# Kernel optimization log

Hardware: AMD Instinct MI355X
Metric: run time of the kernel (lower is better)

## Reference

```python
import jax, jax.numpy as jnp
import numpy as np

B, T, S_ENC, D = 2, 1024, 1024, 2048
NQ, NKV, H = 16, 8, 256
EPS = 1e-6
CAP = 50.0
SCALE = 0.0625  # query_pre_attn_scalar = head_dim**-0.5
BASE = 10000
K_MASK = -2.3819763e+38


def rms_norm(x, scale, eps=EPS):
    var = jnp.mean(jnp.square(x), axis=-1, keepdims=True)
    return x * jax.lax.rsqrt(var + eps) * (1.0 + scale)


def apply_rope(x, positions, base=BASE):
    # x: [B, L, N, H], positions: [B, L] float. rope_proportion=1.0 -> full head.
    head_dim = x.shape[-1]
    timescale = base ** (2.0 / head_dim * jnp.arange(head_dim // 2, dtype=jnp.float32))
    sinusoid = positions[..., None] / timescale  # [B, L, H/2]
    sinusoid = sinusoid[..., None, :]            # [B, L, 1, H/2]
    sin, cos = jnp.sin(sinusoid), jnp.cos(sinusoid)
    x1, x2 = jnp.split(x, 2, axis=-1)
    return jnp.concatenate([x1 * cos - x2 * sin, x2 * cos + x1 * sin], axis=-1).astype(x.dtype)


def setup_inputs() -> dict:
    key = jax.random.key(0)
    ks = jax.random.split(key, 6)
    hidden_states = jax.random.normal(ks[0], (B, T, D), jnp.float32)
    encoder_hidden_states = jax.random.normal(ks[1], (B, S_ENC, D), jnp.float32)
    position_ids = jnp.broadcast_to(jnp.arange(T, dtype=jnp.int32), (B, T))
    causal = jnp.tril(jnp.ones((T, T), bool))
    merged = jnp.concatenate([causal, jnp.ones((T, S_ENC), bool)], axis=-1)
    merged_attention_mask = jnp.broadcast_to(merged[None, None], (B, 1, T, T + S_ENC))
    q_w = jax.random.normal(ks[2], (NQ, D, H), jnp.float32) * 0.02
    k_w = jax.random.normal(ks[3], (NKV, D, H), jnp.float32) * 0.02
    v_w = jax.random.normal(ks[4], (NKV, D, H), jnp.float32) * 0.02
    o_w = jax.random.normal(ks[5], (NQ, H, D), jnp.float32) * 0.02
    q_scale = jnp.zeros((H,), jnp.float32)
    k_scale = jnp.zeros((H,), jnp.float32)
    return {
        'hidden_states': hidden_states,
        'encoder_hidden_states': encoder_hidden_states,
        'position_ids': position_ids,
        'merged_attention_mask': merged_attention_mask,
        'q_w': q_w, 'k_w': k_w, 'v_w': v_w, 'o_w': o_w,
        'q_scale': q_scale, 'k_scale': k_scale,
    }


def reference(hidden_states, encoder_hidden_states, position_ids, merged_attention_mask,
              q_w, k_w, v_w, o_w, q_scale, k_scale):
    # Fused QKV projections
    q = jnp.einsum('BTD,NDH->BTNH', hidden_states, q_w)
    self_k = jnp.einsum('BTD,NDH->BTNH', hidden_states, k_w)
    self_v = jnp.einsum('BTD,NDH->BTNH', hidden_states, v_w)
    # QK RMSNorm
    q = rms_norm(q, q_scale)
    self_k = rms_norm(self_k, k_scale)
    # RoPE on decoder-side q/k only
    pos = position_ids.astype(jnp.float32)
    q = apply_rope(q, pos)
    self_k = apply_rope(self_k, pos)
    # Cross KV (no RoPE, k-norm applied)
    cross_k = rms_norm(jnp.einsum('BTD,NDH->BTNH', encoder_hidden_states, k_w), k_scale)
    cross_v = jnp.einsum('BTD,NDH->BTNH', encoder_hidden_states, v_w)
    # Merge KV: [B, T+S_enc, NKV, H]
    k = jnp.concatenate([self_k, cross_k], axis=1)
    v = jnp.concatenate([self_v, cross_v], axis=1)
    q = q * SCALE
    # GQA: group query heads over kv heads
    G = NQ // NKV
    qg = q.reshape(B, T, NKV, G, H)
    logits = jnp.einsum('BTKGH,BSKH->BKGTS', qg, k)
    # Logit soft-cap
    logits = CAP * jnp.tanh(logits / CAP)
    mask = merged_attention_mask[:, 0][:, None, None]  # [B,1,1,T,S_comb]
    logits = jnp.where(mask, logits, K_MASK)
    probs = jax.nn.softmax(logits, axis=-1)
    out = jnp.einsum('BKGTS,BSKH->BTKGH', probs, v).reshape(B, T, NQ, H)
    return jnp.einsum('BTNH,NHD->BTD', out, o_w)
```

## Files before the change

### kernel.cpp

```cpp
#include <hip/hip_runtime.h>
#include <hip/hip_bf16.h>
#include <stdint.h>

typedef __hip_bfloat16 bf16;
typedef __attribute__((ext_vector_type(8))) short bv8;
typedef __attribute__((ext_vector_type(4))) float f32x4;


__device__ __forceinline__ f32x4 mfma16(bv8 a, bv8 b, f32x4 c) {
  return __builtin_amdgcn_mfma_f32_16x16x32_bf16(a, b, c, 0, 0, 0);
}

__device__ __forceinline__ void gload16(const void* g, void* lds) {
  __builtin_amdgcn_global_load_lds((const __attribute__((address_space(1))) void*)g,
                                   (__attribute__((address_space(3))) void*)lds, 16, 0, 0);
}

__device__ __forceinline__ void storeC(float* p, float v) { *p = v; }
__device__ __forceinline__ void storeC(bf16* p, float v) { *p = __float2bfloat16(v); }

__global__ void cast2_f32_bf16(const float* __restrict__ a, const float* __restrict__ b,
                               bf16* __restrict__ da, bf16* __restrict__ db, int n4each) {
  int i = blockIdx.x * blockDim.x + threadIdx.x;
  const float* s;
  bf16* d;
  if (i < n4each) { s = a; d = da; }
  else            { s = b; d = db; i -= n4each; }
  float4 v = reinterpret_cast<const float4*>(s)[i];
  bf16 t[4] = {__float2bfloat16(v.x), __float2bfloat16(v.y),
               __float2bfloat16(v.z), __float2bfloat16(v.w)};
  reinterpret_cast<uint64_t*>(d)[i] = *reinterpret_cast<uint64_t*>(t);
}

__global__ void transpose_all(const float* __restrict__ q_w, const float* __restrict__ k_w,
                              const float* __restrict__ v_w, const float* __restrict__ o_w,
                              bf16* __restrict__ wqkvt, bf16* __restrict__ owt) {
  __shared__ float tile[32][33];
  const int bid = blockIdx.x;
  const float* s;
  bf16* d;
  int R, C, c0, r0;
  if (bid < 16384) {
    const int z = bid >> 9;
    const int rem = bid & 511;
    s = (z < 16) ? q_w + (size_t)z * 524288
      : (z < 24) ? k_w + (size_t)(z - 16) * 524288
                 : v_w + (size_t)(z - 24) * 524288;
    d = wqkvt + (size_t)z * 524288;
    R = 2048; C = 256;
    c0 = (rem & 7) * 32; r0 = (rem >> 3) * 32;
  } else {
    const int rem = bid - 16384;
    s = o_w; d = owt;
    R = 4096; C = 2048;
    c0 = (rem & 63) * 32; r0 = (rem >> 6) * 32;
  }
  const int x = threadIdx.x, y = threadIdx.y;
#pragma unroll
  for (int i = 0; i < 32; i += 8)
    tile[y + i][x] = s[(size_t)(r0 + y + i) * C + c0 + x];
  __syncthreads();
#pragma unroll
  for (int i = 0; i < 32; i += 8)
    d[(size_t)(c0 + y + i) * R + r0 + x] = __float2bfloat16(tile[x][y + i]);
}

__global__ void transpose_v2(const bf16* __restrict__ vself, const bf16* __restrict__ vcross,
                             bf16* __restrict__ dst) {
  __shared__ bf16 tile[32][33];
  const int z = blockIdx.z;
  const int zz = z & 15, b = zz >> 3, kvh = zz & 7;
  const bool cross = z >= 16;
  const bf16* srcb = cross ? vcross : vself;
  const int src_ld = cross ? 4096 : 8192;
  const int t0 = cross ? 1024 : 0;
  const bf16* s = srcb + (size_t)(b * 1024) * src_ld + kvh * 256;
  bf16* d = dst + (size_t)(zz * 256) * 2048 + t0;
  const int h0 = blockIdx.x * 32, tt0 = blockIdx.y * 32;
  const int x = threadIdx.x, y = threadIdx.y;
#pragma unroll
  for (int i = 0; i < 32; i += 8)
    tile[y + i][x] = s[(size_t)(tt0 + y + i) * src_ld + h0 + x];
  __syncthreads();
#pragma unroll
  for (int i = 0; i < 32; i += 8)
    d[(size_t)(h0 + y + i) * 2048 + tt0 + x] = tile[x][y + i];
}

template <typename CT>
__device__ __forceinline__ void gemm_body(const bf16* __restrict__ A, const bf16* __restrict__ Bt,
                                          CT* __restrict__ C, int N, int K,
                                          int m0, int n0, int kbase, int ksteps) {
  __shared__ __align__(16) bf16 As[128 * 32];
  __shared__ __align__(16) bf16 Bs[128 * 32];
  const int tid = threadIdx.x;
  const int w = tid >> 6, l = tid & 63;
  const int wr = w >> 1, wc = w & 1;
  const int l15 = l & 15, lhi = l >> 4;
  const bf16* ag = A + (size_t)(m0 + (tid >> 2)) * K + kbase + (tid & 3) * 8;
  const bf16* bg = Bt + (size_t)(n0 + (tid >> 2)) * K + kbase + (tid & 3) * 8;
  bf16* asw = As + w * 512;
  bf16* bsw = Bs + w * 512;
  f32x4 acc[4][4] = {};
  for (int k0 = 0; k0 < ksteps; k0 += 32) {
    gload16(ag + k0, asw);
    gload16(ag + (size_t)64 * K + k0, asw + 2048);
    gload16(bg + k0, bsw);
    gload16(bg + (size_t)64 * K + k0, bsw + 2048);
    asm volatile("s_waitcnt vmcnt(0)" ::: "memory");
    __syncthreads();
    bv8 af[4], bfv[4];
#pragma unroll
    for (int m = 0; m < 4; ++m)
      af[m] = *reinterpret_cast<const bv8*>(As + (wr * 64 + m * 16 + l15) * 32 + lhi * 8);
#pragma unroll
    for (int n = 0; n < 4; ++n)
      bfv[n] = *reinterpret_cast<const bv8*>(Bs + (wc * 64 + n * 16 + l15) * 32 + lhi * 8);
#pragma unroll
    for (int m = 0; m < 4; ++m)
#pragma unroll
      for (int n = 0; n < 4; ++n)
        acc[m][n] = mfma16(af[m], bfv[n], acc[m][n]);
    __syncthreads();
  }
  const int r0 = m0 + wr * 64 + lhi * 4;
  const int c0 = n0 + wc * 64 + l15;
#pragma unroll
  for (int m = 0; m < 4; ++m)
#pragma unroll
    for (int n = 0; n < 4; ++n) {
      f32x4 v = acc[m][n];
#pragma unroll
      for (int j = 0; j < 4; ++j)
        storeC(&C[(size_t)(r0 + m * 16 + j) * N + c0 + n * 16], v[j]);
    }
}

__launch_bounds__(256)
__global__ void gemm_proj(const bf16* __restrict__ hid, const bf16* __restrict__ enc,
                          const bf16* __restrict__ wqkvt, bf16* __restrict__ cself,
                          bf16* __restrict__ ccross) {
  const int bx = blockIdx.x;
  const bool cross = bx >= 64;
  const bf16* A = cross ? enc : hid;
  const bf16* Bt = cross ? wqkvt + 8388608 : wqkvt;
  bf16* C = cross ? ccross : cself;
  const int N = cross ? 4096 : 8192;
  const int n0 = (cross ? bx - 64 : bx) * 128;
  gemm_body<bf16>(A, Bt, C, N, 2048, blockIdx.y * 128, n0, 0, 2048);
}

__launch_bounds__(256)
__global__ void gemm_osplit(const bf16* __restrict__ A, const bf16* __restrict__ Bt,
                            float* __restrict__ out, float* __restrict__ p1,
                            float* __restrict__ p2, float* __restrict__ p3) {
  const int z = blockIdx.z;
  float* C = (z == 0) ? out : (z == 1) ? p1 : (z == 2) ? p2 : p3;
  gemm_body<float>(A, Bt, C, 2048, 4096, blockIdx.y * 128, blockIdx.x * 128,
                   z * 1024, 1024);
}

__global__ void add_inplace4(float* __restrict__ out, const float* __restrict__ p1,
                             const float* __restrict__ p2, const float* __restrict__ p3,
                             int n4) {
  int i = blockIdx.x * blockDim.x + threadIdx.x;
  if (i >= n4) return;
  float4 a = reinterpret_cast<float4*>(out)[i];
  float4 b = reinterpret_cast<const float4*>(p1)[i];
  float4 c = reinterpret_cast<const float4*>(p2)[i];
  float4 d = reinterpret_cast<const float4*>(p3)[i];
  a.x += b.x + c.x + d.x;
  a.y += b.y + c.y + d.y;
  a.z += b.z + c.z + d.z;
  a.w += b.w + c.w + d.w;
  reinterpret_cast<float4*>(out)[i] = a;
}

__launch_bounds__(256)
__global__ void norm_all(const bf16* __restrict__ cself, const bf16* __restrict__ ccross,
                         const float* __restrict__ q_s, const float* __restrict__ k_s,
                         const int* __restrict__ pos_ids,
                         bf16* __restrict__ qb, bf16* __restrict__ kbuf) {
  const int rid = blockIdx.x * 4 + (threadIdx.x >> 6);
  const int l = threadIdx.x & 63;
  const bf16* src;
  const float* scale;
  bf16* dst;
  int r, src_ld, src_col0, nheads, dst_S, dst_t0;
  float mul;
  bool rope;
  if (rid < 32768) {
    r = rid; src = cself; src_ld = 8192; src_col0 = 0; scale = q_s;
    dst = qb; nheads = 16; dst_S = 1024; dst_t0 = 0; mul = 0.0625f; rope = true;
  } else if (rid < 49152) {
    r = rid - 32768; src = cself; src_ld = 8192; src_col0 = 4096; scale = k_s;
    dst = kbuf; nheads = 8; dst_S = 2048; dst_t0 = 0; mul = 1.0f; rope = true;
  } else {
    r = rid - 49152; src = ccross; src_ld = 4096; src_col0 = 0; scale = k_s;
    dst = kbuf; nheads = 8; dst_S = 2048; dst_t0 = 1024; mul = 1.0f; rope = false;
  }
  const int token = r / nheads;
  const int n = r - token * nheads;
  const int b = token >> 10;
  const int t = token & 1023;
  const size_t soff = (size_t)token * src_ld + src_col0 + n * 256 + l * 4;
  bf16 xb[4];
  *reinterpret_cast<uint64_t*>(xb) = *reinterpret_cast<const uint64_t*>(src + soff);
  float x[4];
#pragma unroll
  for (int c = 0; c < 4; ++c) x[c] = __bfloat162float(xb[c]);
  float ss = x[0] * x[0] + x[1] * x[1] + x[2] * x[2] + x[3] * x[3];
#pragma unroll
  for (int d = 1; d < 64; d <<= 1) ss += __shfl_xor(ss, d);
  const float rr = rsqrtf(ss * (1.0f / 256.0f) + 1e-6f);
  float v[4];
#pragma unroll
  for (int c = 0; c < 4; ++c) v[c] = x[c] * rr * (1.0f + scale[l * 4 + c]);
  if (rope) {
    const float pos = (float)pos_ids[token];
    float o[4];
#pragma unroll
    for (int c = 0; c < 4; ++c) {
      const int j = (l & 31) * 4 + c;
      const float inv_ts = exp2f(-(float)j * 0.10381025296523007f);
      const float arg = pos * inv_ts;
      const float sj = sinf(arg), cj = cosf(arg);
      const float partner = __shfl_xor(v[c], 32);
      o[c] = (l < 32) ? (v[c] * cj - partner * sj) : (v[c] * cj + partner * sj);
    }
#pragma unroll
    for (int c = 0; c < 4; ++c) v[c] = o[c];
  }
  bf16 ob[4];
#pragma unroll
  for (int c = 0; c < 4; ++c) ob[c] = __float2bfloat16(v[c] * mul);
  const size_t doff = ((size_t)((b * nheads + n) * dst_S + dst_t0 + t)) * 256 + l * 4;
  *reinterpret_cast<uint64_t*>(dst + doff) = *reinterpret_cast<uint64_t*>(ob);
}

__launch_bounds__(512, 2)
__global__ void attn_kernel(const bf16* __restrict__ qb, const bf16* __restrict__ kb,
                            const bf16* __restrict__ vt, bf16* __restrict__ attn_out) {
  __shared__ __align__(16) bf16 Ks[2][64 * 256];
  __shared__ __align__(16) bf16 Vs[2][256 * 64];
  __shared__ __align__(16) bf16 pbuf[2][64 * 72];
  __shared__ float rsb[2][4][2][4][4];
  const int lin = blockIdx.x + 16 * blockIdx.y;
  const int kvc = (lin & 7) | (((lin >> 7) & 1) << 3);
  const int p   = (lin >> 3) & 15;
  const int b = kvc >> 3, kvh = kvc & 7;
  const int tid = threadIdx.x, w = tid >> 6, l = tid & 63;
  const int g = w >> 2, i2 = (w >> 1) & 1, sh = w & 1, hq = w & 3;
  const int n = kvh * 2 + g;
  const int l15 = l & 15, lhi = l >> 4;
  const int xr = (l15 & 7) << 4;

  const int rA = p * 32, rB = (31 - p) * 32;
  const int ntSelf = ((31 - p) >> 1) + 1;
  const int nASelf = (p >> 1) + 1;
  const int nt = ntSelf + 16;

  const bf16* kbase = kb + (size_t)(b * 8 + kvh) * 2048 * 256;
  const bf16* vbase = vt + (size_t)(b * 8 + kvh) * 256 * 2048;

  const bf16* ksrc[4];
  const bf16* vsrc[4];
#pragma unroll
  for (int i = 0; i < 4; ++i) {
    const int r0 = (w * 4 + i) * 2 + (l >> 5);
    const int cbs = ((l & 31) * 16) ^ ((r0 & 7) << 4);
    ksrc[i] = kbase + r0 * 256 + (cbs >> 1);
    const int h0 = (w * 4 + i) * 8 + (l >> 3);
    const int cbv = ((l & 7) * 16) ^ ((h0 & 7) << 4);
    vsrc[i] = vbase + (size_t)h0 * 2048 + (cbv >> 1);
  }

  bv8 qf[2][8];
#pragma unroll
  for (int h = 0; h < 2; ++h) {
    const int rbase = (h ? rB : rA) + i2 * 16;
    const bf16* qp = qb + ((size_t)(b * 16 + n) * 1024 + rbase + l15) * 256 + lhi * 8;
#pragma unroll
    for (int f = 0; f < 8; ++f) qf[h][f] = *reinterpret_cast<const bv8*>(qp + f * 32);
  }

  f32x4 oacc[4][4] = {};
  float rs[2][4] = {};

#pragma unroll
  for (int i = 0; i < 4; ++i) gload16(ksrc[i], &Ks[0][(w * 4 + i) * 512]);
#pragma unroll
  for (int i = 0; i < 4; ++i) gload16(vsrc[i], &Vs[0][(w * 4 + i) * 512]);
  asm volatile("s_waitcnt vmcnt(0)" ::: "memory");
  __syncthreads();

  for (int it = 0; it < nt; ++it) {
    const int cur = it & 1;
    const int s0 = (it < ntSelf) ? it * 64 : 1024 + (it - ntSelf) * 64;
    const bool selfpart = it < ntSelf;
    const bool aAct = (it < nASelf) || !selfpart;
    if (it + 1 < nt) {
      const int itn = it + 1;
      const int s1 = (itn < ntSelf) ? itn * 64 : 1024 + (itn - ntSelf) * 64;
#pragma unroll
      for (int i = 0; i < 4; ++i)
        gload16(ksrc[i] + (size_t)s1 * 256, &Ks[cur ^ 1][(w * 4 + i) * 512]);
#pragma unroll
      for (int i = 0; i < 4; ++i)
        gload16(vsrc[i] + s1, &Vs[cur ^ 1][(w * 4 + i) * 512]);
    }
    f32x4 lacc[2][2] = {};
    __builtin_amdgcn_s_setprio(1);
#pragma unroll
    for (int ss2 = 0; ss2 < 2; ++ss2) {
      const int rbase = ((sh * 2 + ss2) * 16 + l15) * 256;
#pragma unroll
      for (int f = 0; f < 8; ++f) {
        const int off = rbase + (((f * 64 + lhi * 16) ^ xr) >> 1);
        bv8 kf = *reinterpret_cast<const bv8*>(&Ks[cur][off]);
        lacc[1][ss2] = mfma16(qf[1][f], kf, lacc[1][ss2]);
        if (aAct) lacc[0][ss2] = mfma16(qf[0][f], kf, lacc[0][ss2]);
      }
    }
    __builtin_amdgcn_s_setprio(0);
#pragma unroll
    for (int h = 0; h < 2; ++h) {
      if (h == 0 && !aAct) continue;
      const int slot = h ? (i2 + 2) : i2;
      const int rbase = (h ? rB : rA) + i2 * 16;
#pragma unroll
      for (int ss2 = 0; ss2 < 2; ++ss2)
#pragma unroll
        for (int j = 0; j < 4; ++j) {
          const float raw = lacc[h][ss2][j];
          const float e2 = __expf(raw * 0.04f);
          const int s_idx = s0 + (sh * 2 + ss2) * 16 + l15;
          const int trow = rbase + lhi * 4 + j;
          const bool ok = !selfpart || (s_idx <= trow);
          const float pv = ok ? __expf(50.f - __fdividef(100.f, e2 + 1.f)) : 0.f;
          rs[h][j] += pv;
          pbuf[g][(slot * 16 + lhi * 4 + j) * 72 + (sh * 2 + ss2) * 16 + l15] =
              __float2bfloat16(pv);
        }
    }
    __syncthreads();
    __builtin_amdgcn_s_setprio(1);
#pragma unroll
    for (int ks = 0; ks < 2; ++ks) {
      bv8 paB[2], paA[2];
#pragma unroll
      for (int q = 0; q < 2; ++q)
        paB[q] = *reinterpret_cast<const bv8*>(
            &pbuf[g][((2 + q) * 16 + l15) * 72 + ks * 32 + lhi * 8]);
      if (aAct)
#pragma unroll
        for (int q = 0; q < 2; ++q)
          paA[q] = *reinterpret_cast<const bv8*>(
              &pbuf[g][(q * 16 + l15) * 72 + ks * 32 + lhi * 8]);
#pragma unroll
      for (int i = 0; i < 4; ++i) {
        const int off = ((hq * 4 + i) * 16 + l15) * 64 + (((ks * 64 + lhi * 16) ^ xr) >> 1);
        bv8 vf = *reinterpret_cast<const bv8*>(&Vs[cur][off]);
        oacc[2][i] = mfma16(paB[0], vf, oacc[2][i]);
        oacc[3][i] = mfma16(paB[1], vf, oacc[3][i]);
        if (aAct) {
          oacc[0][i] = mfma16(paA[0], vf, oacc[0][i]);
          oacc[1][i] = mfma16(paA[1], vf, oacc[1][i]);
        }
      }
    }
    __builtin_amdgcn_s_setprio(0);
    asm volatile("s_waitcnt vmcnt(0)" ::: "memory");
    __syncthreads();
  }
#pragma unroll
  for (int h = 0; h < 2; ++h) {
    const int slot = h ? (i2 + 2) : i2;
#pragma unroll
    for (int j = 0; j < 4; ++j) {
      float s = rs[h][j];
      s += __shfl_xor(s, 1);
      s += __shfl_xor(s, 2);
      s += __shfl_xor(s, 4);
      s += __shfl_xor(s, 8);
      if (l15 == 0) rsb[g][slot][sh][j][lhi] = s;
    }
  }
  __syncthreads();
  const int rowb[4] = {rA, rA + 16, rB, rB + 16};
  bf16* op = attn_out + (size_t)(b * 1024) * 4096 + n * 256 + l15;
#pragma unroll
  for (int slot = 0; slot < 4; ++slot) {
    float invr[4];
#pragma unroll
    for (int j = 0; j < 4; ++j)
      invr[j] = 1.0f / (rsb[g][slot][0][j][lhi] + rsb[g][slot][1][j][lhi]);
#pragma unroll
    for (int i = 0; i < 4; ++i)
#pragma unroll
      for (int j = 0; j < 4; ++j)
        op[(size_t)(rowb[slot] + lhi * 4 + j) * 4096 + (hq * 4 + i) * 16] =
            __float2bfloat16(oacc[slot][i][j] * invr[j]);
  }
}

extern "C" void kernel_launch(void* const* d_in, const int* in_sizes, int n_in,
                              void* d_out, int out_size, void* d_ws, size_t ws_size,
                              hipStream_t stream) {
  (void)in_sizes; (void)n_in; (void)out_size; (void)ws_size;
  const float* hidden = (const float*)d_in[0];
  const float* enc    = (const float*)d_in[1];
  const int*   pos    = (const int*)d_in[2];
  const float* q_w = (const float*)d_in[4];
  const float* k_w = (const float*)d_in[5];
  const float* v_w = (const float*)d_in[6];
  const float* o_w = (const float*)d_in[7];
  const float* q_s = (const float*)d_in[8];
  const float* k_s = (const float*)d_in[9];
  float* out = (float*)d_out;

  char* base = (char*)d_ws;
  bf16* hid_b  = (bf16*)(base + 0);
  bf16* enc_b  = (bf16*)(base + 8388608);
  bf16* qb     = (bf16*)(base + 0);
  float* p2    = (float*)(base + 0);
  bf16* wqkvt  = (bf16*)(base + 16777216);
  bf16* kbuf   = (bf16*)(base + 16777216);
  float* p3    = (float*)(base + 16777216);
  bf16* vtb    = (bf16*)(base + 33554432);
  bf16* owt    = (bf16*)(base + 50331648);
  bf16* cself  = (bf16*)(base + 67108864);
  bf16* attn_b = (bf16*)(base + 67108864);
  float* p1    = (float*)(base + 83886080);
  bf16* ccross = (bf16*)(base + 100663296);

  dim3 tb32(32, 8);
  cast2_f32_bf16<<<8192, 256, 0, stream>>>(hidden, enc, hid_b, enc_b, 1048576);
  transpose_all<<<24576, tb32, 0, stream>>>(q_w, k_w, v_w, o_w, wqkvt, owt);
  gemm_proj<<<dim3(96, 16), 256, 0, stream>>>(hid_b, enc_b, wqkvt, cself, ccross);
  norm_all<<<16384, 256, 0, stream>>>(cself, ccross, q_s, k_s, pos, qb, kbuf);
  transpose_v2<<<dim3(8, 32, 32), tb32, 0, stream>>>(cself + 6144, ccross + 2048, vtb);
  attn_kernel<<<dim3(16, 16), 512, 0, stream>>>(qb, kbuf, vtb, attn_b);
  gemm_osplit<<<dim3(16, 16, 4), 256, 0, stream>>>(attn_b, owt, out, p1, p2, p3);
  add_inplace4<<<4096, 256, 0, stream>>>(out, p1, p2, p3, 1048576);
}
```

Baseline: 367.5 us.

## Replace projection GEMM with 256x256-tile pipelined kernel and XCD-aware block mapping

Replaces the 128x128-tile QKV projection GEMM with a 256x256-tile, 512-thread kernel. It double-buffers A and B tiles in swizzled LDS using direct global-to-LDS loads, and interleaves the B prefetch with the MFMA sub-phases under manual waitcnt, barriers and s_setprio. Block indices are remapped so each XCD works on a contiguous group of N tiles. The goal is more reuse per loaded byte and better L2 locality across XCDs, at the cost of more registers and LDS per block and fragile hand-written synchronisation.

```diff
diff --git a/kernel.cpp b/kernel.cpp
--- a/kernel.cpp
+++ b/kernel.cpp
@@ -136,18 +136,121 @@
     }
 }
 
-__launch_bounds__(256)
-__global__ void gemm_proj(const bf16* __restrict__ hid, const bf16* __restrict__ enc,
-                          const bf16* __restrict__ wqkvt, bf16* __restrict__ cself,
-                          bf16* __restrict__ ccross) {
-  const int bx = blockIdx.x;
-  const bool cross = bx >= 64;
-  const bf16* A = cross ? enc : hid;
-  const bf16* Bt = cross ? wqkvt + 8388608 : wqkvt;
-  bf16* C = cross ? ccross : cself;
-  const int N = cross ? 4096 : 8192;
-  const int n0 = (cross ? bx - 64 : bx) * 128;
-  gemm_body<bf16>(A, Bt, C, N, 2048, blockIdx.y * 128, n0, 0, 2048);
+__device__ __forceinline__ void stage_half(const bf16* __restrict__ G, int ldg, int row0,
+                                           int kcol0, bf16* lds, int tid) {
+#pragma unroll
+  for (int j = 0; j < 2; ++j) {
+    const int idx = tid + j * 512;
+    const int r = idx >> 3;
+    const int cb = ((idx & 7) * 16) ^ ((r & 7) << 4);
+    gload16(G + (size_t)(row0 + r) * ldg + kcol0 + (cb >> 1), lds + idx * 8);
+  }
+}
+
+__device__ __forceinline__ bv8 frag(const bf16* p, int row, int ks, int lhi, int xw) {
+  return *reinterpret_cast<const bv8*>(p + row * 64 + (((ks * 64 + lhi * 16) ^ xw) >> 1));
+}
+
+__launch_bounds__(512, 2)
+__global__ void gemm_proj256(const bf16* __restrict__ hid, const bf16* __restrict__ enc,
+                             const bf16* __restrict__ wqkvt, bf16* __restrict__ cself,
+                             bf16* __restrict__ ccross) {
+  __shared__ __align__(16) bf16 Al[2][2][128 * 64];
+  __shared__ __align__(16) bf16 Bl[2][2][128 * 64];
+  const int lin = blockIdx.x;
+  const int xcd = lin & 7, idx = lin >> 3;
+  const bf16* A;
+  const bf16* Bt;
+  bf16* C;
+  int N, M0, N0;
+  if (idx < 32) {
+    A = hid; Bt = wqkvt; C = cself; N = 8192;
+    M0 = (idx >> 2) * 256; N0 = (xcd * 4 + (idx & 3)) * 256;
+  } else {
+    const int u = idx - 32;
+    A = enc; Bt = wqkvt + 8388608; C = ccross; N = 4096;
+    M0 = (u >> 1) * 256; N0 = (xcd * 2 + (u & 1)) * 256;
+  }
+  const int K = 2048, T = 32;
+  const int tid = threadIdx.x, w = tid >> 6, l = tid & 63;
+  const int wm = w >> 2, wn = w & 3;
+  const int l15 = l & 15, lhi = l >> 4;
+  const int xw = (l15 & 7) << 4;
+
+  f32x4 acc[8][4] = {};
+
+  stage_half(A, K, M0, 0, Al[0][0], tid);
+  stage_half(A, K, M0 + 128, 0, Al[0][1], tid);
+  stage_half(Bt, K, N0, 0, Bl[0][0], tid);
+  stage_half(Bt, K, N0 + 128, 0, Bl[0][1], tid);
+  stage_half(Bt, K, N0, 64, Bl[1][0], tid);
+  stage_half(Bt, K, N0 + 128, 64, Bl[1][1], tid);
+
+  for (int t = 0; t < T; ++t) {
+    const int d = t & 1;
+    const bf16* Ab = Al[d][wm];
+    const bf16* Bb = Bl[d][wn >> 1];
+    const int rb0 = (wn & 1) * 64;
+    const int k1 = (((t + 1) < T) ? (t + 1) : 0) * 64;
+    const int k2 = (((t + 2) < T) ? (t + 2) : 0) * 64;
+    stage_half(A, K, M0, k1, Al[d ^ 1][0], tid);
+    stage_half(A, K, M0 + 128, k1, Al[d ^ 1][1], tid);
+    asm volatile("s_waitcnt vmcnt(8)" ::: "memory");
+    asm volatile("s_barrier" ::: "memory");
+    bv8 bfr[4][2];
+#pragma unroll
+    for (int i = 0; i < 4; ++i)
+#pragma unroll
+      for (int ks = 0; ks < 2; ++ks)
+        bfr[i][ks] = frag(Bb, rb0 + i * 16 + l15, ks, lhi, xw);
+    {
+      bv8 af[2][2];
+#pragma unroll
+      for (int mm = 0; mm < 2; ++mm)
+#pragma unroll
+        for (int ks = 0; ks < 2; ++ks) af[mm][ks] = frag(Ab, mm * 16 + l15, ks, lhi, xw);
+      __builtin_amdgcn_s_setprio(1);
+#pragma unroll
+      for (int ks = 0; ks < 2; ++ks)
+#pragma unroll
+        for (int mm = 0; mm < 2; ++mm)
+#pragma unroll
+          for (int i = 0; i < 4; ++i)
+            acc[mm][i] = mfma16(af[mm][ks], bfr[i][ks], acc[mm][i]);
+      __builtin_amdgcn_s_setprio(0);
+    }
+    asm volatile("s_barrier" ::: "memory");
+#pragma unroll
+    for (int q = 1; q < 4; ++q) {
+      bv8 af[2][2];
+#pragma unroll
+      for (int mm = 0; mm < 2; ++mm)
+#pragma unroll
+        for (int ks = 0; ks < 2; ++ks)
+          af[mm][ks] = frag(Ab, (q * 2 + mm) * 16 + l15, ks, lhi, xw);
+      if (q == 1) stage_half(Bt, K, N0, k2, Bl[d][0], tid);
+      if (q == 2) stage_half(Bt, K, N0 + 128, k2, Bl[d][1], tid);
+      __builtin_amdgcn_s_setprio(1);
+#pragma unroll
+      for (int ks = 0; ks < 2; ++ks)
+#pragma unroll
+        for (int mm = 0; mm < 2; ++mm)
+#pragma unroll
+          for (int i = 0; i < 4; ++i)
+            acc[q * 2 + mm][i] = mfma16(af[mm][ks], bfr[i][ks], acc[q * 2 + mm][i]);
+      __builtin_amdgcn_s_setprio(0);
+      asm volatile("s_barrier" ::: "memory");
+    }
+  }
+  const int r0 = M0 + wm * 128 + lhi * 4;
+  const int c0 = N0 + wn * 64 + l15;
+#pragma unroll
+  for (int m = 0; m < 8; ++m)
+#pragma unroll
+    for (int i = 0; i < 4; ++i)
+#pragma unroll
+      for (int j = 0; j < 4; ++j)
+        C[(size_t)(r0 + m * 16 + j) * N + c0 + i * 16] = __float2bfloat16(acc[m][i][j]);
 }
 
 __launch_bounds__(256)
@@ -437,7 +540,7 @@
   dim3 tb32(32, 8);
   cast2_f32_bf16<<<8192, 256, 0, stream>>>(hidden, enc, hid_b, enc_b, 1048576);
   transpose_all<<<24576, tb32, 0, stream>>>(q_w, k_w, v_w, o_w, wqkvt, owt);
-  gemm_proj<<<dim3(96, 16), 256, 0, stream>>>(hid_b, enc_b, wqkvt, cself, ccross);
+  gemm_proj256<<<384, 512, 0, stream>>>(hid_b, enc_b, wqkvt, cself, ccross);
   norm_all<<<16384, 256, 0, stream>>>(cself, ccross, q_s, k_s, pos, qb, kbuf);
   transpose_v2<<<dim3(8, 32, 32), tb32, 0, stream>>>(cself + 6144, ccross + 2048, vtb);
   attn_kernel<<<dim3(16, 16), 512, 0, stream>>>(qb, kbuf, vtb, attn_b);
```

After: 418.2 us. 13.8% more time.
